# Kernel tuning notes

Measured on AMD Instinct MI355X. Metric: run time of the kernel, lower is better.

Reference implementation:

```python
import jax, jax.numpy as jnp
import numpy as np


def _local_indices(H, W, K):
    # KxK local window per pixel; border neighbors clamped to the image (replicate padding)
    half = K // 2
    d = np.arange(-half, half + 1)
    r = np.clip(np.arange(H)[:, None, None, None] + d[None, None, :, None], 0, H - 1)
    c = np.clip(np.arange(W)[None, :, None, None] + d[None, None, None, :], 0, W - 1)
    return (r * W + c).reshape(H * W, K * K).astype(np.int32)


def setup_inputs():
    B, C, H, W = 2, 32, 128, 128
    K, S = 25, 1024
    N = H * W
    k1, k2, k3, k4 = jax.random.split(jax.random.key(0), 4)
    key_feat = jax.random.normal(k1, (B, C, H, W), dtype=jnp.float32)
    query_feat = jax.random.normal(k2, (B, C, H, W), dtype=jnp.float32)
    segment_target = jax.random.randint(k3, (B, 1, H, W), 0, 64, dtype=jnp.int32)
    local = jnp.broadcast_to(jnp.asarray(_local_indices(H, W, K))[None], (B, N, K * K))
    rand_glob = jax.random.randint(k4, (B, N, S - K * K), 0, N, dtype=jnp.int32)
    sample_inds = jnp.concatenate([local, rand_glob], axis=-1)  # [B, N, S]
    return {"key_feat": key_feat, "query_feat": query_feat,
            "segment_target": segment_target, "sample_inds": sample_inds}


def _affinity_logits(key_f, query_f, sample_inds, chunk=1024):
    # key_f, query_f: [B, N, C]; sample_inds: [B, N, S]
    B, N, C = key_f.shape
    S = sample_inds.shape[-1]
    nchunks = N // chunk
    q_c = query_f.reshape(B, nchunks, chunk, C).transpose(1, 0, 2, 3)
    i_c = sample_inds.reshape(B, nchunks, chunk, S).transpose(1, 0, 2, 3)

    def body(carry, args):
        q, idx = args                                   # [B, chunk, C], [B, chunk, S]
        kg = jax.vmap(lambda kb, ib: kb[ib])(key_f, idx)  # [B, chunk, S, C]
        return carry, jnp.einsum('bnsc,bnc->bns', kg, q)

    _, lc = jax.lax.scan(body, None, (q_c, i_c))        # [nchunks, B, chunk, S]
    logits = lc.transpose(1, 0, 2, 3).reshape(B, N, S)
    return logits * (C ** -0.5)


def _loss(logits, sample_inds, segment_target):
    B, N, S = logits.shape
    seg = segment_target.reshape(B, N)
    samples = jax.vmap(lambda s, i: s[i])(seg, sample_inds)      # [B, N, S]
    targets = (seg[:, :, None] == samples).astype(logits.dtype)
    mask = (seg != 0).astype(logits.dtype)[:, :, None]           # [B, N, 1]
    # weighted_softmax(logits, mask)
    xe = jnp.exp(logits - jnp.max(logits, -1, keepdims=True))
    denom = jnp.sum(xe * mask, -1, keepdims=True)
    y_prob = xe * mask / (denom + 1e-9)
    y_pred = jnp.log(jnp.clip(y_prob, 1e-8, None))
    y_true = targets / (jnp.sum(targets, -1, keepdims=True) + 1e-9)
    # F.kl_div(y_pred, y_true, reduction='none') with 0*log(0) = 0
    kl = jnp.where(y_true > 0,
                   y_true * (jnp.log(jnp.clip(y_true, 1e-30, None)) - y_pred),
                   0.0) * mask
    agg_mask = (jnp.sum(mask, -1) > 0).astype(logits.dtype)
    return jnp.sum(kl) / (jnp.sum(agg_mask) + 1e-9)


def reference(key_feat, query_feat, segment_target, sample_inds):
    B, C, H, W = key_feat.shape
    N = H * W
    key_f = key_feat.reshape(B, C, N).transpose(0, 2, 1)    # [B, N, C]
    query_f = query_feat.reshape(B, C, N).transpose(0, 2, 1)
    logits = _affinity_logits(key_f, query_f, sample_inds)  # [B, N, S], scaled by C**-0.5
    loss = _loss(logits, sample_inds, segment_target)
    return (logits, loss)
```

## Files before the change

kernel.cpp:

```cpp
#include <hip/hip_runtime.h>
#include <stdint.h>

typedef _Float16 h2 __attribute__((ext_vector_type(2)));
typedef _Float16 h4 __attribute__((ext_vector_type(4)));
typedef float    f4 __attribute__((ext_vector_type(4)));

static constexpr int CDIM = 32;
static constexpr int NPIX = 16384;
static constexpr int SSAM = 1024;
static constexpr int NLOC = 625;
static constexpr int NRND = SSAM - NLOC;
static constexpr int ROWS_PER_BLOCK = 16;

__device__ __forceinline__ uint16_t f2h(float f) {
    union { _Float16 h; uint16_t u; } c;
    c.h = (_Float16)f;
    return c.u;
}

template<int CTRL>
__device__ __forceinline__ float dpp_add(float x) {
    int y = __builtin_amdgcn_mov_dpp(__float_as_int(x), CTRL, 0xF, 0xF, true);
    return x + __int_as_float(y);
}

__device__ __forceinline__ float dot2(h2 a, h2 b, float c) {
    return __builtin_amdgcn_fdot2(a, b, c, false);
}

__global__ __launch_bounds__(256)
void prep_kernel(const float* __restrict__ key_f,
                 const float* __restrict__ query_f,
                 const int* __restrict__ seg32,
                 uint8_t* __restrict__ key16,
                 uint8_t* __restrict__ q16,
                 uint8_t* __restrict__ seg8,
                 uint32_t* __restrict__ segbit,
                 int N, int rows, float scale)
{
    int gI = blockIdx.x * 256 + threadIdx.x;
    if (gI >= rows) return;
    segbit[2 * gI]     = 0;
    segbit[2 * gI + 1] = 0;
    seg8[gI] = (uint8_t)seg32[gI];

    int b = gI / N, n = gI - b * N;
    const size_t cb = (size_t)b * CDIM;

    uint32_t kp[16], qp[16];
#pragma unroll
    for (int c = 0; c < CDIM; c += 2) {
        float k0 = key_f[(cb + c) * N + n];
        float k1 = key_f[(cb + c + 1) * N + n];
        float q0 = query_f[(cb + c) * N + n] * scale;
        float q1 = query_f[(cb + c + 1) * N + n] * scale;
        kp[c >> 1] = (uint32_t)f2h(k0) | ((uint32_t)f2h(k1) << 16);
        qp[c >> 1] = (uint32_t)f2h(q0) | ((uint32_t)f2h(q1) << 16);
    }
    uint4* ko = (uint4*)(key16 + ((size_t)gI << 6));
    uint4* qo = (uint4*)(q16 + ((size_t)gI << 6));
#pragma unroll
    for (int j = 0; j < 4; ++j) {
        ko[j] = make_uint4(kp[4*j], kp[4*j+1], kp[4*j+2], kp[4*j+3]);
        qo[j] = make_uint4(qp[4*j], qp[4*j+1], qp[4*j+2], qp[4*j+3]);
    }
}

__global__ __launch_bounds__(256)
void segbit_build(const int* __restrict__ seg32,
                  uint32_t* __restrict__ segbit,
                  int N, int rows)
{
    int g = blockIdx.x * 256 + threadIdx.x;
    if (g >= rows) return;
    int b = g / N, n = g - b * N;
    int v = seg32[g] & 63;
    atomicOr(&segbit[(((size_t)(b * 64 + v)) << 9) + (n >> 5)], 1u << (n & 31));
}

__global__ __launch_bounds__(256)
void dense_local(const uint8_t* __restrict__ key16,
                 const uint8_t* __restrict__ q16,
                 const uint8_t* __restrict__ seg8,
                 float* __restrict__ out,
                 float* __restrict__ zA,
                 float* __restrict__ tA,
                 float* __restrict__ slA)
{
    const int tid  = threadIdx.x;
    const int bid  = blockIdx.x;
    const int b    = bid >> 8;
    const int t8   = bid & 255;
    const int y0   = (t8 >> 4) << 3;
    const int x0   = (t8 & 15) << 3;
    const int lane = tid & 63;
    const int w    = tid >> 6;

    __shared__ __align__(16) uint8_t  kslot[256 * 80];
    __shared__ __align__(16) _Float16 res[4][16][256];
    __shared__ uint8_t wseg[1024];
    __shared__ float   rowacc[4][16][3];

    const uint8_t* kb = key16 + ((size_t)b << 20);
    const uint8_t* sb = seg8 + ((size_t)b << 14);
    const int yo = y0 - 12, xo = x0 - 12;

    for (int s = tid; s < 1024; s += 256) {
        int i = s >> 5, j = s & 31;
        int yy = min(max(yo + i, 0), 127);
        int xx = min(max(xo + j, 0), 127);
        wseg[s] = sb[(yy << 7) + xx];
    }
    if (tid < 192) ((float*)rowacc)[tid] = 0.f;

    const int qsel = (w << 4) + (lane & 15);
    const int qyA  = qsel >> 3, qxA = qsel & 7;
    const size_t qrow = ((size_t)b << 14) + ((size_t)(y0 + qyA) << 7) + (x0 + qxA);
    const int koff = (lane >> 4) << 3;
    const h4 a0 = *(const h4*)(q16 + (qrow << 6) + koff);
    const h4 a1 = *(const h4*)(q16 + (qrow << 6) + 32 + koff);

    __syncthreads();

    for (int t = 0; t < 4; ++t) {
        for (int s = tid; s < 1024; s += 256) {
            int slot = s >> 2, q = s & 3;
            int i = (t << 3) + (slot >> 5), j = slot & 31;
            int yy = min(max(yo + i, 0), 127);
            int xx = min(max(xo + j, 0), 127);
            *(uint4*)(kslot + slot * 80 + (q << 4)) =
                *(const uint4*)(kb + ((((size_t)(yy << 7)) + xx) << 6) + (q << 4));
        }
        __syncthreads();

#pragma unroll 4
        for (int n = 0; n < 16; ++n) {
            const uint8_t* kr = kslot + ((n << 4) + (lane & 15)) * 80;
            h4 b0 = *(const h4*)(kr + koff);
            h4 b1 = *(const h4*)(kr + 32 + koff);
            f4 acc = {0.f, 0.f, 0.f, 0.f};
            acc = __builtin_amdgcn_mfma_f32_16x16x16f16(a0, b0, acc, 0, 0, 0);
            acc = __builtin_amdgcn_mfma_f32_16x16x16f16(a1, b1, acc, 0, 0, 0);
#pragma unroll
            for (int r = 0; r < 4; ++r)
                res[w][((lane >> 4) << 2) + r][(n << 4) + (lane & 15)] =
                    (_Float16)acc[r];
        }

        for (int m = 0; m < 16; ++m) {
            const int q  = (w << 4) + m;
            const int qy = q >> 3, qx = q & 7;
            const int row = (b << 14) + ((y0 + qy) << 7) + (x0 + qx);
            const int segr = (int)wseg[((qy + 12) << 5) + qx + 12];
            int sLo = ((t << 3) - qy) * 25; if (sLo < 0) sLo = 0;
            int sHi = ((t << 3) - qy + 8) * 25; if (sHi > NLOC) sHi = NLOC;
            float z = 0.f, tc = 0.f, sl = 0.f;
            for (int s = sLo + lane; s < sHi; s += 64) {
                int d25 = (s * 5243) >> 17;
                int r25 = s - d25 * 25;
                int i  = qy + d25;
                int wc = qx + r25;
                float v = (float)res[w][m][((i - (t << 3)) << 5) + wc];
                out[((size_t)row << 10) + s] = v;
                z += __expf(v);
                if ((int)wseg[(i << 5) + wc] == segr) { tc += 1.f; sl += v; }
            }
#pragma unroll
            for (int off = 32; off >= 1; off >>= 1) {
                z  += __shfl_xor(z,  off, 64);
                tc += __shfl_xor(tc, off, 64);
                sl += __shfl_xor(sl, off, 64);
            }
            if (lane == 0) {
                rowacc[w][m][0] += z;
                rowacc[w][m][1] += tc;
                rowacc[w][m][2] += sl;
            }
        }
        __syncthreads();
    }

    if (tid < 64) {
        int q = tid, qy = q >> 3, qx = q & 7;
        int row = (b << 14) + ((y0 + qy) << 7) + (x0 + qx);
        zA[row]  = rowacc[q >> 4][q & 15][0];
        tA[row]  = rowacc[q >> 4][q & 15][1];
        slA[row] = rowacc[q >> 4][q & 15][2];
    }
}

__global__ __launch_bounds__(256)
void affinity_rand(const int* __restrict__ inds,
                   const uint8_t* __restrict__ key16,
                   const uint8_t* __restrict__ q16,
                   const int* __restrict__ seg32,
                   const uint32_t* __restrict__ segbit,
                   const float* __restrict__ zA,
                   const float* __restrict__ tA,
                   const float* __restrict__ slA,
                   float* __restrict__ out,
                   float* __restrict__ ws_kl)
{
    const int tid  = threadIdx.x;
    const int row0 = blockIdx.x * ROWS_PER_BLOCK;
    const int b    = row0 >> 14;
    const int lane = tid & 63;
    const int w    = tid >> 6;
    const int g    = lane >> 2;
    const int sub  = lane & 3;
    const int gidx = (w << 4) + g;

    __shared__ __align__(16) int      idx_lds[2][448];
    __shared__ __align__(16) uint32_t bm_lds[2][512];
    __shared__ float red[2][3][4];
    __shared__ float zp[ROWS_PER_BLOCK], tp[ROWS_PER_BLOCK], sp[ROWS_PER_BLOCK];

    const uint32_t* sbase_bm = segbit + ((size_t)(b * 64) << 9);

    if (tid < ROWS_PER_BLOCK)           zp[tid] = zA[row0 + tid];
    else if (tid < 2*ROWS_PER_BLOCK)    tp[tid - ROWS_PER_BLOCK] = tA[row0 + tid - ROWS_PER_BLOCK];
    else if (tid < 3*ROWS_PER_BLOCK)    sp[tid - 2*ROWS_PER_BLOCK] = slA[row0 + tid - 2*ROWS_PER_BLOCK];

    {
        const int* ib = inds + ((size_t)row0 << 10) + NLOC;
        idx_lds[0][tid] = ib[tid];
        if (tid < NRND - 256) idx_lds[0][256 + tid] = ib[256 + tid];
    }
    int scur = seg32[row0];
    ((uint2*)bm_lds[0])[tid] =
        ((const uint2*)(sbase_bm + ((size_t)(scur & 63) << 9)))[tid];
    uint4 qcur = *(const uint4*)(q16 + ((size_t)row0 << 6) + (sub << 4));
    __syncthreads();

    const uint8_t* kb = key16 + ((size_t)b << 20);
    const uint32_t subs = (uint32_t)(sub << 4);
    const bool act6 = (384 + gidx) < NRND;

    for (int r = 0; r < ROWS_PER_BLOCK; ++r) {
        const int row = row0 + r;
        const int p   = r & 1;
        const int* cur = idx_lds[p];
        const bool hasNext = (r + 1 < ROWS_PER_BLOCK);

        h2 qh0, qh1, qh2, qh3;
        {
            union { uint4 u; h2 h[4]; } qc; qc.u = qcur;
            qh0 = qc.h[0]; qh1 = qc.h[1]; qh2 = qc.h[2]; qh3 = qc.h[3];
        }
        const int seg_n = scur;

        int idxs[7];
#pragma unroll
        for (int i = 0; i < 7; ++i)
            idxs[i] = cur[(i << 6) + gidx];

        uint4 kd[7];
#pragma unroll
        for (int i = 0; i < 6; ++i)
            kd[i] = *(const uint4*)(kb + (((uint32_t)idxs[i] << 6) | subs));
        kd[6] = make_uint4(0, 0, 0, 0);
        if (act6)
            kd[6] = *(const uint4*)(kb + (((uint32_t)idxs[6] << 6) | subs));

        int pre0 = 0, pre1 = 0; uint4 qnext; uint2 pre_bm; int snext;
        if (hasNext) {
            const int* ib = inds + ((size_t)(row + 1) << 10) + NLOC;
            pre0 = ib[tid];
            if (tid < NRND - 256) pre1 = ib[256 + tid];
            qnext  = *(const uint4*)(q16 + ((size_t)(row + 1) << 6) + (sub << 4));
            snext  = seg32[row + 1];
            pre_bm = ((const uint2*)(sbase_bm + ((size_t)(snext & 63) << 9)))[tid];
        }
        const bool owned1 = (sub < 2) || (sub == 2 && act6);
        int tfm = 0;
        {
            int idx0 = cur[(sub << 6) + gidx];
            if ((bm_lds[p][idx0 >> 5] >> (idx0 & 31)) & 1u) tfm |= 1;
            if (sub < 3) {
                int idx1 = cur[((sub + 4) << 6) + gidx];
                if (owned1 && ((bm_lds[p][idx1 >> 5] >> (idx1 & 31)) & 1u))
                    tfm |= 2;
            }
        }

        const size_t obase = ((size_t)row << 10) + NLOC;
        float lg0 = 0.f, lg1 = 0.f;
#pragma unroll
        for (int it = 0; it < 7; ++it) {
            union { uint4 u; h2 h[4]; } kc; kc.u = kd[it];
            float acc = dot2(kc.h[0], qh0, 0.f);
            acc = dot2(kc.h[1], qh1, acc);
            acc = dot2(kc.h[2], qh2, acc);
            acc = dot2(kc.h[3], qh3, acc);
            acc = dpp_add<0xB1>(acc);
            acc = dpp_add<0x4E>(acc);
            if (sub == (it & 3)) {
                if (it < 4) lg0 = acc;
                else        lg1 = acc;
                if (it < 6 || act6)
                    out[obase + (it << 6) + gidx] = acc;
            }
        }

        float z  = __expf(lg0) + (owned1 ? __expf(lg1) : 0.f);
        float tc = (float)__popc((unsigned)tfm);
        float sl = ((tfm & 1) ? lg0 : 0.f) + ((tfm & 2) ? lg1 : 0.f);
#pragma unroll
        for (int off = 32; off >= 1; off >>= 1) {
            z  += __shfl_xor(z,  off, 64);
            tc += __shfl_xor(tc, off, 64);
            sl += __shfl_xor(sl, off, 64);
        }
        if (lane == 0) {
            red[p][0][w] = z;
            red[p][1][w] = tc;
            red[p][2][w] = sl;
        }

        if (hasNext) {
            idx_lds[p ^ 1][tid] = pre0;
            if (tid < NRND - 256) idx_lds[p ^ 1][256 + tid] = pre1;
            ((uint2*)bm_lds[p ^ 1])[tid] = pre_bm;
            qcur = qnext;
            scur = snext;
        }
        __syncthreads();

        if (tid == 0) {
            if (seg_n != 0) {
                const float Z  = zp[r] + (red[p][0][0] + red[p][0][1]) + (red[p][0][2] + red[p][0][3]);
                const float T  = tp[r] + (red[p][1][0] + red[p][1][1]) + (red[p][1][2] + red[p][1][3]);
                const float SL = sp[r] + (red[p][2][0] + red[p][2][1]) + (red[p][2][2] + red[p][2][3]);
                ws_kl[row] = -__logf(T) - SL / T + __logf(Z);
            } else {
                ws_kl[row] = 0.f;
            }
        }
    }
}

__global__ __launch_bounds__(256)
void affinity_fallback(const float* __restrict__ key_f,
                       const float* __restrict__ query_f,
                       const int*   __restrict__ seg32,
                       const int*   __restrict__ inds,
                       float* __restrict__ out,
                       float* __restrict__ ws_kl,
                       int N, int S, float scale)
{
    const int bid = blockIdx.x;
    const int tid = threadIdx.x;
    const int b   = bid / N;

    __shared__ float q_lds[CDIM];
    __shared__ float redA[4], redB[4], redC[4];

    if (tid < CDIM) {
        int n = bid - b * N;
        q_lds[tid] = query_f[((size_t)(b * CDIM + tid)) * N + n];
    }
    const int seg_n = seg32[bid];
    __syncthreads();

    float q[CDIM];
#pragma unroll
    for (int c = 0; c < CDIM; ++c) q[c] = q_lds[c];

    const size_t rowbase = (size_t)bid * S;
    const int4 iv = ((const int4*)(inds + rowbase))[tid];
    const int idxv[4] = {iv.x, iv.y, iv.z, iv.w};

    float lg[4];
    int   tf[4];
#pragma unroll
    for (int k = 0; k < 4; ++k) {
        int idx = idxv[k];
        tf[k] = (seg32[b * N + idx] == seg_n) ? 1 : 0;
        float acc = 0.f;
#pragma unroll
        for (int c = 0; c < CDIM; ++c)
            acc = fmaf(key_f[((size_t)(b * CDIM + c)) * N + idx], q[c], acc);
        lg[k] = acc * scale;
    }
    ((float4*)(out + rowbase))[tid] = make_float4(lg[0], lg[1], lg[2], lg[3]);

    const int lane = tid & 63, wv = tid >> 6;
    float m = fmaxf(fmaxf(lg[0], lg[1]), fmaxf(lg[2], lg[3]));
#pragma unroll
    for (int off = 32; off >= 1; off >>= 1)
        m = fmaxf(m, __shfl_xor(m, off, 64));
    if (lane == 0) redA[wv] = m;
    __syncthreads();
    m = fmaxf(fmaxf(redA[0], redA[1]), fmaxf(redA[2], redA[3]));

    float e[4], z = 0.f, tcnt = 0.f;
#pragma unroll
    for (int k = 0; k < 4; ++k) {
        e[k] = expf(lg[k] - m);
        z += e[k];
        tcnt += (float)tf[k];
    }
#pragma unroll
    for (int off = 32; off >= 1; off >>= 1) {
        z    += __shfl_xor(z, off, 64);
        tcnt += __shfl_xor(tcnt, off, 64);
    }
    if (lane == 0) { redB[wv] = z; redC[wv] = tcnt; }
    __syncthreads();
    const float Z = redB[0] + redB[1] + redB[2] + redB[3];
    const float T = redC[0] + redC[1] + redC[2] + redC[3];

    float kl = 0.f;
    if (seg_n != 0) {
        const float invZ = 1.f / (Z + 1e-9f);
        const float invT = 1.f / (T + 1e-9f);
        const float nlT  = -logf(T + 1e-9f);
#pragma unroll
        for (int k = 0; k < 4; ++k) {
            if (tf[k]) {
                float p = e[k] * invZ;
                float yp = logf(fmaxf(p, 1e-8f));
                kl += invT * (nlT - yp);
            }
        }
    }
#pragma unroll
    for (int off = 32; off >= 1; off >>= 1)
        kl += __shfl_xor(kl, off, 64);
    if (lane == 0) redA[wv] = kl;
    __syncthreads();
    if (tid == 0)
        ws_kl[bid] = redA[0] + redA[1] + redA[2] + redA[3];
}

__global__ __launch_bounds__(1024)
void loss_reduce(const float* __restrict__ ws_kl,
                 const int* __restrict__ seg32,
                 float* __restrict__ out_loss, int rows)
{
    const int tid = threadIdx.x;
    float s = 0.f, c = 0.f;
    for (int i = tid; i < rows; i += 1024) {
        s += ws_kl[i];
        c += (seg32[i] != 0) ? 1.f : 0.f;
    }
#pragma unroll
    for (int off = 32; off >= 1; off >>= 1) {
        s += __shfl_xor(s, off, 64);
        c += __shfl_xor(c, off, 64);
    }
    __shared__ float sA[16], sB[16];
    const int lane = tid & 63, wv = tid >> 6;
    if (lane == 0) { sA[wv] = s; sB[wv] = c; }
    __syncthreads();
    if (tid == 0) {
        float ts = 0.f, tc = 0.f;
#pragma unroll
        for (int k = 0; k < 16; ++k) { ts += sA[k]; tc += sB[k]; }
        out_loss[0] = ts / (tc + 1e-9f);
    }
}

extern "C" void kernel_launch(void* const* d_in, const int* in_sizes, int n_in,
                              void* d_out, int out_size, void* d_ws, size_t ws_size,
                              hipStream_t stream)
{
    const float* key_f   = (const float*)d_in[0];
    const float* query_f = (const float*)d_in[1];
    const int*   seg32   = (const int*)d_in[2];
    const int*   inds    = (const int*)d_in[3];
    float* out = (float*)d_out;

    const int N    = NPIX;
    const int rows = in_sizes[2];
    const int S    = in_sizes[3] / rows;
    const float scale = (float)(1.0 / sqrt((double)CDIM));
    const int B    = rows / N;

    const size_t off_q16 = (size_t)rows * 64;
    const size_t off_s8  = off_q16 + (size_t)rows * 64;
    const size_t off_sb  = (off_s8 + (size_t)rows + 255) & ~(size_t)255;
    const size_t sb_words = (size_t)B * 64 * 512;
    const size_t off_zA  = (off_sb + sb_words * 4 + 255) & ~(size_t)255;
    const size_t off_tA  = off_zA + (size_t)rows * 4;
    const size_t off_slA = off_tA + (size_t)rows * 4;
    const size_t off_kl  = off_slA + (size_t)rows * 4;
    const size_t need    = off_kl + (size_t)rows * 4;

    uint8_t* wsb = (uint8_t*)d_ws;
    const bool geom_ok = (S == SSAM) && (rows % N == 0) &&
                         (rows % ROWS_PER_BLOCK == 0);

    if (ws_size >= need && geom_ok) {
        uint8_t*  key16  = wsb;
        uint8_t*  q16    = wsb + off_q16;
        uint8_t*  seg8   = wsb + off_s8;
        uint32_t* segbit = (uint32_t*)(wsb + off_sb);
        float*    zA     = (float*)(wsb + off_zA);
        float*    tA     = (float*)(wsb + off_tA);
        float*    slA    = (float*)(wsb + off_slA);
        float*    wskl   = (float*)(wsb + off_kl);

        prep_kernel<<<(rows + 255) / 256, 256, 0, stream>>>(
            key_f, query_f, seg32, key16, q16, seg8, segbit, N, rows, scale);
        segbit_build<<<(rows + 255) / 256, 256, 0, stream>>>(
            seg32, segbit, N, rows);
        dense_local<<<B * 256, 256, 0, stream>>>(
            key16, q16, seg8, out, zA, tA, slA);
        affinity_rand<<<rows / ROWS_PER_BLOCK, 256, 0, stream>>>(
            inds, key16, q16, seg32, segbit, zA, tA, slA, out, wskl);
        loss_reduce<<<1, 1024, 0, stream>>>(wskl, seg32, out + (size_t)rows * S, rows);
    } else {
        float* wskl = (float*)d_ws;
        affinity_fallback<<<rows, 256, 0, stream>>>(
            key_f, query_f, seg32, inds, out, wskl, N, S, scale);
        loss_reduce<<<1, 1024, 0, stream>>>(wskl, seg32, out + (size_t)rows * S, rows);
    }
}
```

Baseline: 165.6 us.

## Process two rows per iteration in random-sample kernel to halve barriers

The random-sample loop now handles two query rows per iteration instead of one. LDS buffers for indices and segment bitmaps are doubled, and the prefetch is split across two thread halves. This halves the number of __syncthreads and cross-wave reductions, and doubles the number of independent gathers in flight per thread. The cost is higher register and LDS use, which could reduce occupancy.

```diff
diff --git a/kernel.cpp b/kernel.cpp
--- a/kernel.cpp
+++ b/kernel.cpp
@@ -209,128 +209,178 @@
     const int g    = lane >> 2;
     const int sub  = lane & 3;
     const int gidx = (w << 4) + g;
-
-    __shared__ __align__(16) int      idx_lds[2][448];
-    __shared__ __align__(16) uint32_t bm_lds[2][512];
-    __shared__ float red[2][3][4];
+    const int half = tid >> 7;
+    const int ht   = tid & 127;
+
+    __shared__ __align__(16) int      idx_lds[2][2][448];
+    __shared__ __align__(16) uint32_t bm_lds[2][2][512];
+    __shared__ float red[2][6][4];
     __shared__ float zp[ROWS_PER_BLOCK], tp[ROWS_PER_BLOCK], sp[ROWS_PER_BLOCK];
 
-    const uint32_t* sbase_bm = segbit + ((size_t)(b * 64) << 9);
-
-    if (tid < ROWS_PER_BLOCK)           zp[tid] = zA[row0 + tid];
-    else if (tid < 2*ROWS_PER_BLOCK)    tp[tid - ROWS_PER_BLOCK] = tA[row0 + tid - ROWS_PER_BLOCK];
-    else if (tid < 3*ROWS_PER_BLOCK)    sp[tid - 2*ROWS_PER_BLOCK] = slA[row0 + tid - 2*ROWS_PER_BLOCK];
+    const uint32_t* sbm = segbit + ((size_t)(b * 64) << 9);
+
+    if (tid < ROWS_PER_BLOCK)             zp[tid] = zA[row0 + tid];
+    else if (tid < 2*ROWS_PER_BLOCK)      tp[tid - ROWS_PER_BLOCK] = tA[row0 + tid - ROWS_PER_BLOCK];
+    else if (tid < 3*ROWS_PER_BLOCK)      sp[tid - 2*ROWS_PER_BLOCK] = slA[row0 + tid - 2*ROWS_PER_BLOCK];
 
     {
-        const int* ib = inds + ((size_t)row0 << 10) + NLOC;
-        idx_lds[0][tid] = ib[tid];
-        if (tid < NRND - 256) idx_lds[0][256 + tid] = ib[256 + tid];
-    }
-    int scur = seg32[row0];
-    ((uint2*)bm_lds[0])[tid] =
-        ((const uint2*)(sbase_bm + ((size_t)(scur & 63) << 9)))[tid];
-    uint4 qcur = *(const uint4*)(q16 + ((size_t)row0 << 6) + (sub << 4));
-    __syncthreads();
-
-    const uint8_t* kb = key16 + ((size_t)b << 20);
+        const int* ib = inds + ((size_t)(row0 + half) << 10) + NLOC;
+        idx_lds[0][half][ht]       = ib[ht];
+        idx_lds[0][half][ht + 128] = ib[ht + 128];
+        idx_lds[0][half][ht + 256] = ib[ht + 256];
+        if (ht < NRND - 384)
+            idx_lds[0][half][ht + 384] = ib[ht + 384];
+        int sh = seg32[row0 + half];
+        ((uint4*)bm_lds[0][half])[ht] =
+            ((const uint4*)(sbm + ((size_t)(sh & 63) << 9)))[ht];
+    }
+    int scurA = seg32[row0];
+    int scurB = seg32[row0 + 1];
+    uint4 qcurA = *(const uint4*)(q16 + ((size_t)row0 << 6) + (sub << 4));
+    uint4 qcurB = *(const uint4*)(q16 + ((size_t)(row0 + 1) << 6) + (sub << 4));
+    __syncthreads();
+
+    const uint8_t* kp = key16 + ((size_t)b << 20);
     const uint32_t subs = (uint32_t)(sub << 4);
     const bool act6 = (384 + gidx) < NRND;
-
-    for (int r = 0; r < ROWS_PER_BLOCK; ++r) {
-        const int row = row0 + r;
-        const int p   = r & 1;
-        const int* cur = idx_lds[p];
-        const bool hasNext = (r + 1 < ROWS_PER_BLOCK);
-
-        h2 qh0, qh1, qh2, qh3;
+    const bool owned1 = (sub < 2) || (sub == 2 && act6);
+
+    for (int t = 0; t < ROWS_PER_BLOCK / 2; ++t) {
+        const int rowA = row0 + 2 * t;
+        const int rowB = rowA + 1;
+        const int pp   = t & 1;
+        const int* curA = idx_lds[pp][0];
+        const int* curB = idx_lds[pp][1];
+        const bool hasNext = (t + 1 < ROWS_PER_BLOCK / 2);
+
+        h2 qa0, qa1, qa2, qa3, qb0, qb1, qb2, qb3;
         {
-            union { uint4 u; h2 h[4]; } qc; qc.u = qcur;
-            qh0 = qc.h[0]; qh1 = qc.h[1]; qh2 = qc.h[2]; qh3 = qc.h[3];
-        }
-        const int seg_n = scur;
-
-        int idxs[7];
-#pragma unroll
-        for (int i = 0; i < 7; ++i)
-            idxs[i] = cur[(i << 6) + gidx];
-
-        uint4 kd[7];
-#pragma unroll
-        for (int i = 0; i < 6; ++i)
-            kd[i] = *(const uint4*)(kb + (((uint32_t)idxs[i] << 6) | subs));
-        kd[6] = make_uint4(0, 0, 0, 0);
-        if (act6)
-            kd[6] = *(const uint4*)(kb + (((uint32_t)idxs[6] << 6) | subs));
-
-        int pre0 = 0, pre1 = 0; uint4 qnext; uint2 pre_bm; int snext;
+            union { uint4 u; h2 h[4]; } qc;
+            qc.u = qcurA; qa0 = qc.h[0]; qa1 = qc.h[1]; qa2 = qc.h[2]; qa3 = qc.h[3];
+            qc.u = qcurB; qb0 = qc.h[0]; qb1 = qc.h[1]; qb2 = qc.h[2]; qb3 = qc.h[3];
+        }
+        const int segA = scurA, segB = scurB;
+
+        int ixA[7], ixB[7];
+#pragma unroll
+        for (int i = 0; i < 7; ++i) {
+            ixA[i] = curA[(i << 6) + gidx];
+            ixB[i] = curB[(i << 6) + gidx];
+        }
+
+        uint4 ka[7], kb_[7];
+#pragma unroll
+        for (int i = 0; i < 6; ++i) {
+            ka[i]  = *(const uint4*)(kp + (((uint32_t)ixA[i] << 6) | subs));
+            kb_[i] = *(const uint4*)(kp + (((uint32_t)ixB[i] << 6) | subs));
+        }
+        ka[6] = make_uint4(0, 0, 0, 0);
+        kb_[6] = make_uint4(0, 0, 0, 0);
+        if (act6) {
+            ka[6]  = *(const uint4*)(kp + (((uint32_t)ixA[6] << 6) | subs));
+            kb_[6] = *(const uint4*)(kp + (((uint32_t)ixB[6] << 6) | subs));
+        }
+
+        int pf0 = 0, pf1 = 0, pf2 = 0, pf3 = 0;
+        uint4 bmn; int snA = 0, snB = 0;
+        uint4 qnA, qnB;
         if (hasNext) {
-            const int* ib = inds + ((size_t)(row + 1) << 10) + NLOC;
-            pre0 = ib[tid];
-            if (tid < NRND - 256) pre1 = ib[256 + tid];
-            qnext  = *(const uint4*)(q16 + ((size_t)(row + 1) << 6) + (sub << 4));
-            snext  = seg32[row + 1];
-            pre_bm = ((const uint2*)(sbase_bm + ((size_t)(snext & 63) << 9)))[tid];
-        }
-        const bool owned1 = (sub < 2) || (sub == 2 && act6);
-        int tfm = 0;
+            const int* ibn = inds + ((size_t)(rowA + 2 + half) << 10) + NLOC;
+            pf0 = ibn[ht];
+            pf1 = ibn[ht + 128];
+            pf2 = ibn[ht + 256];
+            if (ht < NRND - 384) pf3 = ibn[ht + 384];
+            snA = seg32[rowA + 2];
+            snB = seg32[rowA + 3];
+            int sh = half ? snB : snA;
+            bmn = ((const uint4*)(sbm + ((size_t)(sh & 63) << 9)))[ht];
+            qnA = *(const uint4*)(q16 + ((size_t)(rowA + 2) << 6) + (sub << 4));
+            qnB = *(const uint4*)(q16 + ((size_t)(rowA + 3) << 6) + (sub << 4));
+        }
+        int tfmA = 0, tfmB = 0;
         {
-            int idx0 = cur[(sub << 6) + gidx];
-            if ((bm_lds[p][idx0 >> 5] >> (idx0 & 31)) & 1u) tfm |= 1;
+            int i0 = curA[(sub << 6) + gidx];
+            if ((bm_lds[pp][0][i0 >> 5] >> (i0 & 31)) & 1u) tfmA |= 1;
+            int i1 = curB[(sub << 6) + gidx];
+            if ((bm_lds[pp][1][i1 >> 5] >> (i1 & 31)) & 1u) tfmB |= 1;
             if (sub < 3) {
-                int idx1 = cur[((sub + 4) << 6) + gidx];
-                if (owned1 && ((bm_lds[p][idx1 >> 5] >> (idx1 & 31)) & 1u))
-                    tfm |= 2;
-            }
-        }
-
-        const size_t obase = ((size_t)row << 10) + NLOC;
-        float lg0 = 0.f, lg1 = 0.f;
+                int j0 = curA[((sub + 4) << 6) + gidx];
+                if (owned1 && ((bm_lds[pp][0][j0 >> 5] >> (j0 & 31)) & 1u)) tfmA |= 2;
+                int j1 = curB[((sub + 4) << 6) + gidx];
+                if (owned1 && ((bm_lds[pp][1][j1 >> 5] >> (j1 & 31)) & 1u)) tfmB |= 2;
+            }
+        }
+
+        const size_t obA = ((size_t)rowA << 10) + NLOC;
+        const size_t obB = ((size_t)rowB << 10) + NLOC;
+        float lgA0 = 0.f, lgA1 = 0.f, lgB0 = 0.f, lgB1 = 0.f;
 #pragma unroll
         for (int it = 0; it < 7; ++it) {
-            union { uint4 u; h2 h[4]; } kc; kc.u = kd[it];
-            float acc = dot2(kc.h[0], qh0, 0.f);
-            acc = dot2(kc.h[1], qh1, acc);
-            acc = dot2(kc.h[2], qh2, acc);
-            acc = dot2(kc.h[3], qh3, acc);
-            acc = dpp_add<0xB1>(acc);
-            acc = dpp_add<0x4E>(acc);
+            union { uint4 u; h2 h[4]; } kc;
+            kc.u = ka[it];
+            float aA = dot2(kc.h[0], qa0, 0.f);
+            aA = dot2(kc.h[1], qa1, aA);
+            aA = dot2(kc.h[2], qa2, aA);
+            aA = dot2(kc.h[3], qa3, aA);
+            kc.u = kb_[it];
+            float aB = dot2(kc.h[0], qb0, 0.f);
+            aB = dot2(kc.h[1], qb1, aB);
+            aB = dot2(kc.h[2], qb2, aB);
+            aB = dot2(kc.h[3], qb3, aB);
+            aA = dpp_add<0xB1>(aA); aA = dpp_add<0x4E>(aA);
+            aB = dpp_add<0xB1>(aB); aB = dpp_add<0x4E>(aB);
             if (sub == (it & 3)) {
-                if (it < 4) lg0 = acc;
-                else        lg1 = acc;
-                if (it < 6 || act6)
-                    out[obase + (it << 6) + gidx] = acc;
-            }
-        }
-
-        float z  = __expf(lg0) + (owned1 ? __expf(lg1) : 0.f);
-        float tc = (float)__popc((unsigned)tfm);
-        float sl = ((tfm & 1) ? lg0 : 0.f) + ((tfm & 2) ? lg1 : 0.f);
+                if (it < 4) { lgA0 = aA; lgB0 = aB; }
+                else        { lgA1 = aA; lgB1 = aB; }
+                if (it < 6 || act6) {
+                    out[obA + (it << 6) + gidx] = aA;
+                    out[obB + (it << 6) + gidx] = aB;
+                }
+            }
+        }
+
+        float z0 = __expf(lgA0) + (owned1 ? __expf(lgA1) : 0.f);
+        float z1 = __expf(lgB0) + (owned1 ? __expf(lgB1) : 0.f);
+        float c0 = (float)__popc((unsigned)tfmA);
+        float c1 = (float)__popc((unsigned)tfmB);
+        float s0 = ((tfmA & 1) ? lgA0 : 0.f) + ((tfmA & 2) ? lgA1 : 0.f);
+        float s1 = ((tfmB & 1) ? lgB0 : 0.f) + ((tfmB & 2) ? lgB1 : 0.f);
 #pragma unroll
         for (int off = 32; off >= 1; off >>= 1) {
-            z  += __shfl_xor(z,  off, 64);
-            tc += __shfl_xor(tc, off, 64);
-            sl += __shfl_xor(sl, off, 64);
+            z0 += __shfl_xor(z0, off, 64);
+            z1 += __shfl_xor(z1, off, 64);
+            c0 += __shfl_xor(c0, off, 64);
+            c1 += __shfl_xor(c1, off, 64);
+            s0 += __shfl_xor(s0, off, 64);
+            s1 += __shfl_xor(s1, off, 64);
         }
         if (lane == 0) {
-            red[p][0][w] = z;
-            red[p][1][w] = tc;
-            red[p][2][w] = sl;
+            red[pp][0][w] = z0; red[pp][1][w] = c0; red[pp][2][w] = s0;
+            red[pp][3][w] = z1; red[pp][4][w] = c1; red[pp][5][w] = s1;
         }
 
         if (hasNext) {
-            idx_lds[p ^ 1][tid] = pre0;
-            if (tid < NRND - 256) idx_lds[p ^ 1][256 + tid] = pre1;
-            ((uint2*)bm_lds[p ^ 1])[tid] = pre_bm;
-            qcur = qnext;
-            scur = snext;
+            idx_lds[pp ^ 1][half][ht]       = pf0;
+            idx_lds[pp ^ 1][half][ht + 128] = pf1;
+            idx_lds[pp ^ 1][half][ht + 256] = pf2;
+            if (ht < NRND - 384) idx_lds[pp ^ 1][half][ht + 384] = pf3;
+            ((uint4*)bm_lds[pp ^ 1][half])[ht] = bmn;
+            qcurA = qnA; qcurB = qnB;
+            scurA = snA; scurB = snB;
         }
         __syncthreads();
 
-        if (tid == 0) {
-            if (seg_n != 0) {
-                const float Z  = zp[r] + (red[p][0][0] + red[p][0][1]) + (red[p][0][2] + red[p][0][3]);
-                const float T  = tp[r] + (red[p][1][0] + red[p][1][1]) + (red[p][1][2] + red[p][1][3]);
-                const float SL = sp[r] + (red[p][2][0] + red[p][2][1]) + (red[p][2][2] + red[p][2][3]);
+        if (tid < 2) {
+            const int  row  = rowA + tid;
+            const int  sgn  = tid ? segB : segA;
+            const int  base = tid * 3;
+            if (sgn != 0) {
+                const float Z  = zp[2*t + tid] +
+                    (red[pp][base][0] + red[pp][base][1]) + (red[pp][base][2] + red[pp][base][3]);
+                const float T  = tp[2*t + tid] +
+                    (red[pp][base+1][0] + red[pp][base+1][1]) + (red[pp][base+1][2] + red[pp][base+1][3]);
+                const float SL = sp[2*t + tid] +
+                    (red[pp][base+2][0] + red[pp][base+2][1]) + (red[pp][base+2][2] + red[pp][base+2][3]);
                 ws_kl[row] = -__logf(T) - SL / T + __logf(Z);
             } else {
                 ws_kl[row] = 0.f;
```

Measured after the change: 165.5 us. Within noise of the previous version (-0.1%).
